# Performance work log

Hardware: AMD Instinct MI355X
Metric: run time of the kernel (lower is better)

Reference implementation:

```python
import jax, jax.numpy as jnp
import numpy as np

D = 256
H = 4
HD = D // H


def rotate_half(x):
    xp = x.reshape(x.shape[:-1] + (-1, 2))
    x1, x2 = xp[..., 0], xp[..., 1]
    return jnp.stack((-x2, x1), axis=-1).reshape(x.shape)


def apply_rope(freqs, t):
    # freqs: [2, B, 1, N, HD]; t: [B, H, N, HD]
    return t * freqs[0] + rotate_half(t) * freqs[1]


def layernorm(x, g, b, eps=1e-5):
    m = jnp.mean(x, axis=-1, keepdims=True)
    v = jnp.var(x, axis=-1, keepdims=True)
    return (x - m) * jax.lax.rsqrt(v + eps) * g + b


def ffn(z, W1, b1, g, be, W2, b2):
    h = layernorm(z @ W1 + b1, g, be)
    h = jax.nn.gelu(h, approximate=False)
    return h @ W2 + b2


def heads_split(t):
    B, N, _ = t.shape
    return t.reshape(B, N, H, HD).transpose(0, 2, 1, 3)  # [B,H,N,HD]


def heads_merge(t):
    B, h, N, hd = t.shape
    return t.transpose(0, 2, 1, 3).reshape(B, N, h * hd)


def sdpa(q, k, v):
    s = q.shape[-1] ** (-0.5)
    sim = jnp.einsum('bhid,bhjd->bhij', q, k) * s
    attn = jax.nn.softmax(sim, axis=-1)
    return jnp.einsum('bhij,bhjd->bhid', attn, v)


def self_block(x, enc, Wqkv, bqkv, Wo, bo, W1, b1, g, be, W2, b2):
    B, N, _ = x.shape
    qkv = (x @ Wqkv + bqkv).reshape(B, N, H, HD, 3).transpose(0, 2, 1, 3, 4)
    q, k, v = qkv[..., 0], qkv[..., 1], qkv[..., 2]
    q = apply_rope(enc, q)
    k = apply_rope(enc, k)
    msg = heads_merge(sdpa(q, k, v)) @ Wo + bo
    return x + ffn(jnp.concatenate([x, msg], axis=-1), W1, b1, g, be, W2, b2)


def cross_block(x0, x1, Wqk, bqk, Wv, bv, Wo, bo, W1, b1, g, be, W2, b2):
    qk0 = heads_split(x0 @ Wqk + bqk)
    qk1 = heads_split(x1 @ Wqk + bqk)
    v0 = heads_split(x0 @ Wv + bv)
    v1 = heads_split(x1 @ Wv + bv)
    s = HD ** (-0.5)
    qk0 = qk0 * (s ** 0.5)
    qk1 = qk1 * (s ** 0.5)
    sim = jnp.einsum('bhid,bhjd->bhij', qk0, qk1)
    attn01 = jax.nn.softmax(sim, axis=-1)
    attn10 = jax.nn.softmax(sim.transpose(0, 1, 3, 2), axis=-1)
    m0 = jnp.einsum('bhij,bhjd->bhid', attn01, v1)
    m1 = jnp.einsum('bhij,bhjd->bhid', attn10, v0)
    m0 = heads_merge(m0) @ Wo + bo
    m1 = heads_merge(m1) @ Wo + bo
    x0 = x0 + ffn(jnp.concatenate([x0, m0], axis=-1), W1, b1, g, be, W2, b2)
    x1 = x1 + ffn(jnp.concatenate([x1, m1], axis=-1), W1, b1, g, be, W2, b2)
    return x0, x1


def setup_inputs() -> dict:
    key = jax.random.key(0)
    ks = jax.random.split(key, 24)
    B, N = 4, 2048
    desc0 = jax.random.normal(ks[0], (B, N, D), jnp.float32)
    desc1 = jax.random.normal(ks[1], (B, N, D), jnp.float32)
    encoding0 = jax.random.uniform(ks[2], (2, B, 1, N, HD), jnp.float32)
    encoding1 = jax.random.uniform(ks[3], (2, B, 1, N, HD), jnp.float32)

    def lin(k, fin, fout):
        k1, k2 = jax.random.split(k)
        W = jax.random.normal(k1, (fin, fout), jnp.float32) * (fin ** -0.5)
        b = jax.random.normal(k2, (fout,), jnp.float32) * 0.01
        return W, b

    Wqkv, bqkv = lin(ks[4], D, 3 * D)
    Wo_s, bo_s = lin(ks[5], D, D)
    W1_s, b1_s = lin(ks[6], 2 * D, 2 * D)
    g_s = jnp.ones((2 * D,), jnp.float32)
    be_s = jnp.zeros((2 * D,), jnp.float32)
    W2_s, b2_s = lin(ks[7], 2 * D, D)
    Wqk_c, bqk_c = lin(ks[8], D, D)
    Wv_c, bv_c = lin(ks[9], D, D)
    Wo_c, bo_c = lin(ks[10], D, D)
    W1_c, b1_c = lin(ks[11], 2 * D, 2 * D)
    g_c = jnp.ones((2 * D,), jnp.float32)
    be_c = jnp.zeros((2 * D,), jnp.float32)
    W2_c, b2_c = lin(ks[12], 2 * D, D)
    return dict(desc0=desc0, desc1=desc1, encoding0=encoding0, encoding1=encoding1,
                Wqkv=Wqkv, bqkv=bqkv, Wo_s=Wo_s, bo_s=bo_s,
                W1_s=W1_s, b1_s=b1_s, g_s=g_s, be_s=be_s, W2_s=W2_s, b2_s=b2_s,
                Wqk_c=Wqk_c, bqk_c=bqk_c, Wv_c=Wv_c, bv_c=bv_c, Wo_c=Wo_c, bo_c=bo_c,
                W1_c=W1_c, b1_c=b1_c, g_c=g_c, be_c=be_c, W2_c=W2_c, b2_c=b2_c)


def reference(desc0, desc1, encoding0, encoding1,
              Wqkv, bqkv, Wo_s, bo_s, W1_s, b1_s, g_s, be_s, W2_s, b2_s,
              Wqk_c, bqk_c, Wv_c, bv_c, Wo_c, bo_c, W1_c, b1_c, g_c, be_c, W2_c, b2_c):
    d0 = self_block(desc0, encoding0, Wqkv, bqkv, Wo_s, bo_s, W1_s, b1_s, g_s, be_s, W2_s, b2_s)
    d1 = self_block(desc1, encoding1, Wqkv, bqkv, Wo_s, bo_s, W1_s, b1_s, g_s, be_s, W2_s, b2_s)
    return cross_block(d0, d1, Wqk_c, bqk_c, Wv_c, bv_c, Wo_c, bo_c, W1_c, b1_c, g_c, be_c, W2_c, b2_c)
```

## Files before the change

### kernel.cpp

```cpp
#include <hip/hip_runtime.h>
#include <math.h>

#define BB 4
#define HH 4
#define NN 2048
#define DD 256
#define HDIM 64
#define NTOK 8192
#define NTOK2 16384

typedef __attribute__((ext_vector_type(8))) __bf16 bf16x8;
typedef __attribute__((ext_vector_type(8))) unsigned short ushort8;
typedef __attribute__((ext_vector_type(4))) float floatx4;
typedef __attribute__((ext_vector_type(4))) short short4v;

union U8 { ushort8 u; bf16x8 b; };
union U4 { unsigned int u[2]; unsigned long long l; short4v s; };

#define MFMA16(a, b, c) __builtin_amdgcn_mfma_f32_16x16x16bf16_1k(a, b, c, 0, 0, 0)

__device__ __forceinline__ unsigned short f2bf(float x) {
    unsigned int u = __float_as_uint(x);
    u += 0x7FFF + ((u >> 16) & 1);
    return (unsigned short)(u >> 16);
}
__device__ __forceinline__ float bf2f(unsigned short u) {
    return __uint_as_float(((unsigned int)u) << 16);
}
__device__ __forceinline__ unsigned int cvtpk(float a, float b) {
    unsigned int r;
    asm("v_cvt_pk_bf16_f32 %0, %1, %2" : "=v"(r) : "v"(a), "v"(b));
    return r;
}
__device__ __forceinline__ floatx4 fmax4(floatx4 a, floatx4 b) {
    floatx4 r;
    r[0] = fmaxf(a[0], b[0]); r[1] = fmaxf(a[1], b[1]);
    r[2] = fmaxf(a[2], b[2]); r[3] = fmaxf(a[3], b[3]);
    return r;
}

struct WTab {
    const float* w[7];
    unsigned short* o[7];
    int K[7];
    int N[7];
    int st[7];
    int t0[8];
};

__global__ __launch_bounds__(256) void wtrans(WTab tab)
{
    __shared__ float lds[32][33];
    const int t = threadIdx.x;
    int bid = blockIdx.x;
    int s = 0;
    while (bid >= tab.t0[s + 1]) s++;
    const int ti = bid - tab.t0[s];
    const int K = tab.K[s], N = tab.N[s], st = tab.st[s];
    const int tx = ti % (N / 32), ty = ti / (N / 32);
    const int k0 = ty * 32, n0 = tx * 32;
    const float* W = tab.w[s];
    unsigned short* Wt = tab.o[s];

    {
        int r = t >> 3, c = (t & 7) * 4;
        float4 a = *(const float4*)&W[(size_t)(k0 + r) * N + n0 + c];
        lds[r][c] = a.x; lds[r][c+1] = a.y; lds[r][c+2] = a.z; lds[r][c+3] = a.w;
    }
    __syncthreads();
    {
        int n = t >> 3, kq = (t & 7) * 4;
        ushort4 p;
        p.x = f2bf(lds[kq+0][n]); p.y = f2bf(lds[kq+1][n]);
        p.z = f2bf(lds[kq+2][n]); p.w = f2bf(lds[kq+3][n]);
        *(ushort4*)&Wt[(size_t)(n0 + n) * st + k0 + kq] = p;
    }
}

__global__ __launch_bounds__(256) void wfuse(
    const float* __restrict__ Wo_s, const float* __restrict__ W1_s,
    unsigned short* __restrict__ o_s,
    const float* __restrict__ Wo_c, const float* __restrict__ W1_c,
    unsigned short* __restrict__ o_c)
{
    __shared__ float wo[32][33];
    __shared__ float w1[32][68];
    const int t = threadIdx.x;
    const int bid = blockIdx.x;
    const int seg = bid >> 6, ti_ = bid & 63;
    const int i0 = (ti_ >> 3) * 32, n0 = (ti_ & 7) * 64;
    const float* Wo  = seg ? Wo_c : Wo_s;
    const float* W1b = (seg ? W1_c : W1_s) + 256 * 512;
    unsigned short* out = seg ? o_c : o_s;
    const int ti = t >> 3, tn = t & 7;

    float acc[8] = {};
    for (int jc = 0; jc < 256; jc += 32) {
        {
            int r = t >> 3, c = (t & 7) * 4;
            *(float4*)&wo[r][c] = *(const float4*)&Wo[(size_t)(i0 + r) * 256 + jc + c];
            int c8 = (t & 7) * 8;
            *(float4*)&w1[r][c8]     = *(const float4*)&W1b[(size_t)(jc + r) * 512 + n0 + c8];
            *(float4*)&w1[r][c8 + 4] = *(const float4*)&W1b[(size_t)(jc + r) * 512 + n0 + c8 + 4];
        }
        __syncthreads();
        #pragma unroll
        for (int j = 0; j < 32; j++) {
            float a = wo[ti][j];
            #pragma unroll
            for (int e = 0; e < 8; e++) acc[e] += a * w1[j][tn * 8 + e];
        }
        __syncthreads();
    }
    #pragma unroll
    for (int e = 0; e < 8; e++)
        out[(size_t)(n0 + tn * 8 + e) * 512 + 256 + i0 + ti] = f2bf(acc[e]);
}

__global__ __launch_bounds__(256) void bfuse(
    const float* bo_s, const float* W1_s, const float* b1_s, float* bs,
    const float* bo_c, const float* W1_c, const float* b1_c, float* bc)
{
    __shared__ float r[4];
    const int bid = blockIdx.x;
    const int seg = bid >> 9, n = bid & 511;
    const float* bo  = seg ? bo_c : bo_s;
    const float* W1b = (seg ? W1_c : W1_s) + 256 * 512;
    const float* b1  = seg ? b1_c : b1_s;
    float* out       = seg ? bc : bs;
    const int j = threadIdx.x;
    float a = bo[j] * W1b[(size_t)j * 512 + n];
    #pragma unroll
    for (int o = 32; o > 0; o >>= 1) a += __shfl_xor(a, o, 64);
    if ((j & 63) == 0) r[j >> 6] = a;
    __syncthreads();
    if (j == 0) out[n] = b1[n] + r[0] + r[1] + r[2] + r[3];
}

__global__ __launch_bounds__(256) void gemm_mfma(
    const unsigned short* __restrict__ A, int lda,
    const unsigned short* __restrict__ Wt, int K,
    const float* __restrict__ bias, const float* __restrict__ bias2, int mode,
    float* outF, unsigned short* outH0, unsigned short* outH1,
    unsigned short* outH2,
    int ldc, const float* R0, const float* R1)
{
    __shared__ __align__(16) unsigned short As[64 * 72];
    __shared__ __align__(16) unsigned short Bs[128 * 72];
    const int t = threadIdx.x;
    const int w = t >> 6, lane = t & 63, quad = lane >> 4, l15 = lane & 15;
    const int m0 = blockIdx.y * 64, n0 = blockIdx.x * 128;
    const int wn = w * 32;
    const int sar = t >> 2, sac = (t & 3) * 16;
    const int sbr = t >> 1, sbc = (t & 1) * 32;

    const unsigned short* Ap = A  + (size_t)(m0 + sar) * lda + sac;
    const unsigned short* Bp = Wt + (size_t)(n0 + sbr) * K   + sbc;

    ushort8 pa0 = *(const ushort8*)(Ap);
    ushort8 pa1 = *(const ushort8*)(Ap + 8);
    ushort8 pb0 = *(const ushort8*)(Bp);
    ushort8 pb1 = *(const ushort8*)(Bp + 8);
    ushort8 pb2 = *(const ushort8*)(Bp + 16);
    ushort8 pb3 = *(const ushort8*)(Bp + 24);

    floatx4 acc[4][2];
    #pragma unroll
    for (int i = 0; i < 4; i++)
        #pragma unroll
        for (int j = 0; j < 2; j++) acc[i][j] = (floatx4){0.f, 0.f, 0.f, 0.f};

    const int nk = K >> 6;
    for (int kk = 0; kk < nk; kk++) {
        *(ushort8*)&As[sar * 72 + sac]      = pa0;
        *(ushort8*)&As[sar * 72 + sac + 8]  = pa1;
        *(ushort8*)&Bs[sbr * 72 + sbc]      = pb0;
        *(ushort8*)&Bs[sbr * 72 + sbc + 8]  = pb1;
        *(ushort8*)&Bs[sbr * 72 + sbc + 16] = pb2;
        *(ushort8*)&Bs[sbr * 72 + sbc + 24] = pb3;
        __syncthreads();
        if (kk + 1 < nk) {
            int ko = (kk + 1) * 64;
            pa0 = *(const ushort8*)(Ap + ko);
            pa1 = *(const ushort8*)(Ap + ko + 8);
            pb0 = *(const ushort8*)(Bp + ko);
            pb1 = *(const ushort8*)(Bp + ko + 8);
            pb2 = *(const ushort8*)(Bp + ko + 16);
            pb3 = *(const ushort8*)(Bp + ko + 24);
        }
        #pragma unroll
        for (int kh = 0; kh < 2; kh++) {
            U8 af[4], bf[2];
            #pragma unroll
            for (int i = 0; i < 4; i++)
                af[i].u = *(const ushort8*)&As[(i * 16 + l15) * 72 + kh * 32 + quad * 8];
            #pragma unroll
            for (int j = 0; j < 2; j++)
                bf[j].u = *(const ushort8*)&Bs[(wn + j * 16 + l15) * 72 + kh * 32 + quad * 8];
            #pragma unroll
            for (int i = 0; i < 4; i++)
                #pragma unroll
                for (int j = 0; j < 2; j++)
                    acc[i][j] = __builtin_amdgcn_mfma_f32_16x16x32_bf16(af[i].b, bf[j].b, acc[i][j], 0, 0, 0);
        }
        __syncthreads();
    }

    #pragma unroll
    for (int i = 0; i < 4; i++) {
        #pragma unroll
        for (int j = 0; j < 2; j++) {
            int col = n0 + wn + j * 16 + l15;
            float bv = (mode == 2 && col >= 256) ? bias2[col & 255] : bias[col];
            #pragma unroll
            for (int r = 0; r < 4; r++) {
                int grow = m0 + i * 16 + quad * 4 + r;
                float v = acc[i][j][r] + bv;
                if (mode == 1) {
                    outH0[(size_t)grow * ldc + col] = f2bf(v);
                } else if (mode == 2) {
                    int cc = col & 255;
                    int h = cc >> 6, d = cc & 63;
                    int ds = grow >> 13, b = (grow >> 11) & 3, n = grow & 2047;
                    int bh = ds * 16 + b * 4 + h;
                    if (col < 256)
                        outH0[((size_t)bh * NN + n) * HDIM + d] = f2bf(v);
                    else
                        outH1[((size_t)bh * HDIM + d) * NN + n] = f2bf(v);
                } else if (mode == 3) {
                    int sel = col % 3, cc = col / 3;
                    int h = cc >> 6, d = cc & 63;
                    int ds = grow >> 13, b = (grow >> 11) & 3, n = grow & 2047;
                    int bh = ds * 16 + b * 4 + h;
                    if (sel == 0)
                        outH0[((size_t)bh * NN + n) * HDIM + d] = f2bf(v);
                    else if (sel == 1)
                        outH1[((size_t)bh * NN + n) * HDIM + d] = f2bf(v);
                    else
                        outH2[((size_t)bh * HDIM + d) * NN + n] = f2bf(v);
                } else {
                    const float* R = (grow < NTOK) ? R0 : R1;
                    float vv = v + R[(size_t)(grow & 8191) * 256 + col];
                    outF[(size_t)grow * 256 + col] = vv;
                    if (outH0) outH0[(size_t)grow * 256 + col] = f2bf(vv);
                    if (outH1) outH1[(size_t)grow * 512 + col] = f2bf(vv);
                }
            }
        }
    }
}

__global__ __launch_bounds__(256) void rope_k(unsigned short* __restrict__ qb,
                                              unsigned short* __restrict__ kb,
                                              const float* __restrict__ enc0,
                                              const float* __restrict__ enc1)
{
    int i = blockIdx.x * 256 + threadIdx.x;
    int dp = (i & 31) * 2;
    int n  = (i >> 5) & (NN - 1);
    int h  = (i >> 16) & 3;
    int b  = (i >> 18) & 3;
    int ds = (i >> 20) & 1;
    int bf = (i >> 21) & 1;
    unsigned short* tq = (bf ? kb : qb) +
        (((size_t)(ds * 16 + b * 4 + h)) * NN + n) * HDIM + dp;
    const float* e0 = (ds ? enc1 : enc0) + ((size_t)b * NN + n) * HDIM + dp;
    const float* e1 = e0 + (size_t)BB * NN * HDIM;
    float x0 = bf2f(tq[0]), x1 = bf2f(tq[1]);
    float y0 = x0 * e0[0] - x1 * e1[0];
    float y1 = x1 * e0[1] + x0 * e1[1];
    tq[0] = f2bf(y0); tq[1] = f2bf(y1);
}

__global__ __launch_bounds__(256) void flash_attn(
    const unsigned short* __restrict__ Q, const unsigned short* __restrict__ K,
    const unsigned short* __restrict__ V, unsigned short* __restrict__ O,
    int ldo, int kvx, float qscale)
{
    __shared__ __align__(16) unsigned short Ks[2][64 * 72];
    __shared__ __align__(16) unsigned short Vt[2][64 * 72];

    const int t    = threadIdx.x;
    const int w    = t >> 6;
    const int lane = t & 63;
    const int quad = lane >> 4;
    const int l15  = lane & 15;
    const int bh   = blockIdx.y;
    const int kbh  = bh ^ kvx;
    const int q0   = blockIdx.x * 128;

    const unsigned short* Qb  = Q + (size_t)bh  * NN * HDIM;
    const unsigned short* Kb  = K + (size_t)kbh * NN * HDIM;
    const unsigned short* VTb = V + (size_t)kbh * NN * HDIM;

    const int srf = t >> 3, scf = (t & 7) * 8;

    bf16x8 qf0[2], qf1[2];
    #pragma unroll
    for (int i = 0; i < 2; i++) {
        const int qrow = q0 + w * 32 + i * 16 + l15;
        U8 r0, r1, x0, x1;
        r0.u = *(const ushort8*)&Qb[(size_t)qrow * HDIM + quad * 8];
        r1.u = *(const ushort8*)&Qb[(size_t)qrow * HDIM + 32 + quad * 8];
        #pragma unroll
        for (int j = 0; j < 8; j++) {
            x0.u[j] = f2bf(bf2f(r0.u[j]) * qscale);
            x1.u[j] = f2bf(bf2f(r1.u[j]) * qscale);
        }
        qf0[i] = x0.b; qf1[i] = x1.b;
    }

    floatx4 o[2][4];
    #pragma unroll
    for (int i = 0; i < 2; i++)
        #pragma unroll
        for (int c = 0; c < 4; c++) o[i][c] = (floatx4){0.f, 0.f, 0.f, 0.f};
    float m[2] = {-1e30f, -1e30f};
    float l[2] = {0.f, 0.f};

    ushort8 ka0 = *(const ushort8*)&Kb[(size_t)srf * HDIM + scf];
    ushort8 ka1 = *(const ushort8*)&Kb[(size_t)(srf + 32) * HDIM + scf];
    ushort8 va0 = *(const ushort8*)&VTb[(size_t)srf * NN + scf];
    ushort8 va1 = *(const ushort8*)&VTb[(size_t)(srf + 32) * NN + scf];
    *(ushort8*)&Ks[0][srf * 72 + scf]        = ka0;
    *(ushort8*)&Ks[0][(srf + 32) * 72 + scf] = ka1;
    *(ushort8*)&Vt[0][srf * 72 + scf]        = va0;
    *(ushort8*)&Vt[0][(srf + 32) * 72 + scf] = va1;
    __syncthreads();

    int cur = 0;
    for (int j0 = 0; j0 < NN; j0 += 64, cur ^= 1) {
        const int more = (j0 + 64 < NN);
        if (more) {
            const int jn = j0 + 64;
            ka0 = *(const ushort8*)&Kb[(size_t)(jn + srf) * HDIM + scf];
            ka1 = *(const ushort8*)&Kb[(size_t)(jn + srf + 32) * HDIM + scf];
            va0 = *(const ushort8*)&VTb[(size_t)srf * NN + jn + scf];
            va1 = *(const ushort8*)&VTb[(size_t)(srf + 32) * NN + jn + scf];
        }

        floatx4 s[2][4];
        __builtin_amdgcn_s_setprio(1);
        #pragma unroll
        for (int t4 = 0; t4 < 4; t4++) {
            U8 k0, k1;
            k0.u = *(const ushort8*)&Ks[cur][(t4 * 16 + l15) * 72 + quad * 8];
            k1.u = *(const ushort8*)&Ks[cur][(t4 * 16 + l15) * 72 + 32 + quad * 8];
            #pragma unroll
            for (int i = 0; i < 2; i++) {
                floatx4 z = (floatx4){0.f, 0.f, 0.f, 0.f};
                z = __builtin_amdgcn_mfma_f32_16x16x32_bf16(k0.b, qf0[i], z, 0, 0, 0);
                z = __builtin_amdgcn_mfma_f32_16x16x32_bf16(k1.b, qf1[i], z, 0, 0, 0);
                s[i][t4] = z;
            }
        }
        __builtin_amdgcn_s_setprio(0);

        short4v pf[2][4];
        #pragma unroll
        for (int i = 0; i < 2; i++) {
            floatx4 a = fmax4(fmax4(s[i][0], s[i][1]), fmax4(s[i][2], s[i][3]));
            float mx = fmaxf(fmaxf(a[0], a[1]), fmaxf(a[2], a[3]));
            mx = fmaxf(mx, __shfl_xor(mx, 16, 64));
            mx = fmaxf(mx, __shfl_xor(mx, 32, 64));
            if (!__all(mx <= m[i] + 8.f)) {
                float mn = fmaxf(m[i], mx);
                float al = exp2f(m[i] - mn);
                m[i] = mn;
                l[i] *= al;
                #pragma unroll
                for (int c = 0; c < 4; c++)
                    #pragma unroll
                    for (int r = 0; r < 4; r++) o[i][c][r] *= al;
            }
            float rs = 0.f;
            #pragma unroll
            for (int t4 = 0; t4 < 4; t4++)
                #pragma unroll
                for (int r = 0; r < 4; r++) {
                    float p = exp2f(s[i][t4][r] - m[i]);
                    s[i][t4][r] = p;
                    rs += p;
                }
            rs += __shfl_xor(rs, 16, 64);
            rs += __shfl_xor(rs, 32, 64);
            l[i] += rs;

            #pragma unroll
            for (int t4 = 0; t4 < 4; t4++) {
                U4 pk;
                pk.u[0] = cvtpk(s[i][t4][0], s[i][t4][1]);
                pk.u[1] = cvtpk(s[i][t4][2], s[i][t4][3]);
                pf[i][t4] = pk.s;
            }
        }

        __builtin_amdgcn_s_setprio(1);
        #pragma unroll
        for (int c = 0; c < 4; c++) {
            U4 vf[4];
            #pragma unroll
            for (int t4 = 0; t4 < 4; t4++)
                vf[t4].l = *(const unsigned long long*)
                    &Vt[cur][(c * 16 + l15) * 72 + t4 * 16 + quad * 4];
            #pragma unroll
            for (int i = 0; i < 2; i++)
                #pragma unroll
                for (int t4 = 0; t4 < 4; t4++)
                    o[i][c] = MFMA16(vf[t4].s, pf[i][t4], o[i][c]);
        }
        __builtin_amdgcn_s_setprio(0);

        if (more) {
            *(ushort8*)&Ks[cur ^ 1][srf * 72 + scf]        = ka0;
            *(ushort8*)&Ks[cur ^ 1][(srf + 32) * 72 + scf] = ka1;
            *(ushort8*)&Vt[cur ^ 1][srf * 72 + scf]        = va0;
            *(ushort8*)&Vt[cur ^ 1][(srf + 32) * 72 + scf] = va1;
            __syncthreads();
        }
    }

    const int ds = bh >> 4, b = (bh >> 2) & 3, h = bh & 3;
    #pragma unroll
    for (int i = 0; i < 2; i++) {
        const int q = q0 + w * 32 + i * 16 + l15;
        const size_t row = (size_t)ds * NTOK + b * NN + q;
        float inv = 1.f / l[i];
        #pragma unroll
        for (int c = 0; c < 4; c++) {
            U4 pk;
            pk.u[0] = cvtpk(o[i][c][0] * inv, o[i][c][1] * inv);
            pk.u[1] = cvtpk(o[i][c][2] * inv, o[i][c][3] * inv);
            *(unsigned long long*)&O[row * ldo + h * HDIM + c * 16 + quad * 4] = pk.l;
        }
    }
}

__global__ __launch_bounds__(256) void ln_gelu(
    unsigned short* __restrict__ hb, const float* __restrict__ g,
    const float* __restrict__ be)
{
    const int lane = threadIdx.x & 63;
    const int wv   = threadIdx.x >> 6;
    const size_t row = (size_t)blockIdx.x * 4 + wv;
    unsigned short* ip = hb + row * 512 + lane * 8;
    U8 v; v.u = *(const ushort8*)ip;
    float x[8];
    float s = 0.f, ss = 0.f;
    #pragma unroll
    for (int j = 0; j < 8; j++) {
        x[j] = bf2f(v.u[j]);
        s += x[j];
        ss += x[j] * x[j];
    }
    #pragma unroll
    for (int o = 32; o > 0; o >>= 1) {
        s  += __shfl_xor(s, o, 64);
        ss += __shfl_xor(ss, o, 64);
    }
    float mean = s * (1.f / 512.f);
    float var  = ss * (1.f / 512.f) - mean * mean;
    float inv  = rsqrtf(var + 1e-5f);
    float4 g0 = *(const float4*)&g[lane * 8];
    float4 g1 = *(const float4*)&g[lane * 8 + 4];
    float4 b0 = *(const float4*)&be[lane * 8];
    float4 b1 = *(const float4*)&be[lane * 8 + 4];
    float gg[8] = {g0.x, g0.y, g0.z, g0.w, g1.x, g1.y, g1.z, g1.w};
    float bb[8] = {b0.x, b0.y, b0.z, b0.w, b1.x, b1.y, b1.z, b1.w};
    #pragma unroll
    for (int j = 0; j < 8; j++) {
        float y = (x[j] - mean) * inv * gg[j] + bb[j];
        v.u[j] = f2bf(0.5f * y * (1.f + erff(y * 0.70710678f)));
    }
    *(ushort8*)ip = v.u;
}

__global__ __launch_bounds__(256) void copy_to_cat(
    const float* __restrict__ s0, const float* __restrict__ s1,
    unsigned short* __restrict__ cat)
{
    int i = blockIdx.x * 256 + threadIdx.x;
    int row = i >> 6, c4 = (i & 63) * 4;
    const float* s = (row < NTOK) ? s0 : s1;
    float4 a = *(const float4*)&s[(size_t)(row & 8191) * 256 + c4];
    ushort4 p = { f2bf(a.x), f2bf(a.y), f2bf(a.z), f2bf(a.w) };
    *(ushort4*)&cat[(size_t)row * 512 + c4] = p;
}

extern "C" void kernel_launch(void* const* d_in, const int* in_sizes, int n_in,
                              void* d_out, int out_size, void* d_ws, size_t ws_size,
                              hipStream_t stream)
{
    const float* desc0 = (const float*)d_in[0];
    const float* desc1 = (const float*)d_in[1];
    const float* enc0  = (const float*)d_in[2];
    const float* enc1  = (const float*)d_in[3];
    const float* Wqkv  = (const float*)d_in[4];  const float* bqkv  = (const float*)d_in[5];
    const float* Wo_s  = (const float*)d_in[6];  const float* bo_s  = (const float*)d_in[7];
    const float* W1_s  = (const float*)d_in[8];  const float* b1_s  = (const float*)d_in[9];
    const float* g_s   = (const float*)d_in[10]; const float* be_s  = (const float*)d_in[11];
    const float* W2_s  = (const float*)d_in[12]; const float* b2_s  = (const float*)d_in[13];
    const float* Wqk_c = (const float*)d_in[14]; const float* bqk_c = (const float*)d_in[15];
    const float* Wv_c  = (const float*)d_in[16]; const float* bv_c  = (const float*)d_in[17];
    const float* Wo_c  = (const float*)d_in[18]; const float* bo_c  = (const float*)d_in[19];
    const float* W1_c  = (const float*)d_in[20]; const float* b1_c  = (const float*)d_in[21];
    const float* g_c   = (const float*)d_in[22]; const float* be_c  = (const float*)d_in[23];
    const float* W2_c  = (const float*)d_in[24]; const float* b2_c  = (const float*)d_in[25];

    char* ws = (char*)d_ws;
    unsigned short* wt  = (unsigned short*)ws;
    unsigned short* qb  = (unsigned short*)(ws + 2490368);
    unsigned short* kb  = (unsigned short*)(ws + 10878976);
    unsigned short* vb  = (unsigned short*)(ws + 27656192);
    unsigned short* cat = (unsigned short*)(ws + 36044800);
    unsigned short* hb  = (unsigned short*)(ws + 52822016);
    unsigned short* dbf = (unsigned short*)(ws + 86376448);

    unsigned short* t_qkv  = wt;
    float*          bias_s = (float*)(wt + 196608);
    unsigned short* t_w1s  = wt + 262144;
    unsigned short* t_w2s  = wt + 524288;
    unsigned short* t_wqkc = wt + 655360;
    float*          bias_c = (float*)(wt + 786432);
    unsigned short* t_w1c  = wt + 851968;
    unsigned short* t_w2c  = wt + 1114112;

    float* outF = (float*)d_out;

    dim3 blk(256);

    WTab tab;
    tab.w[0] = Wqkv;  tab.o[0] = t_qkv;          tab.K[0] = 256; tab.N[0] = 768; tab.st[0] = 256;
    tab.w[1] = W1_s;  tab.o[1] = t_w1s;          tab.K[1] = 256; tab.N[1] = 512; tab.st[1] = 512;
    tab.w[2] = W2_s;  tab.o[2] = t_w2s;          tab.K[2] = 512; tab.N[2] = 256; tab.st[2] = 512;
    tab.w[3] = Wqk_c; tab.o[3] = t_wqkc;         tab.K[3] = 256; tab.N[3] = 256; tab.st[3] = 256;
    tab.w[4] = Wv_c;  tab.o[4] = t_wqkc + 65536; tab.K[4] = 256; tab.N[4] = 256; tab.st[4] = 256;
    tab.w[5] = W1_c;  tab.o[5] = t_w1c;          tab.K[5] = 256; tab.N[5] = 512; tab.st[5] = 512;
    tab.w[6] = W2_c;  tab.o[6] = t_w2c;          tab.K[6] = 512; tab.N[6] = 256; tab.st[6] = 512;
    int acc_t = 0;
    for (int s = 0; s < 7; s++) {
        tab.t0[s] = acc_t;
        acc_t += (tab.K[s] / 32) * (tab.N[s] / 32);
    }
    tab.t0[7] = acc_t;
    hipLaunchKernelGGL(wtrans, dim3(acc_t), blk, 0, stream, tab);
    hipLaunchKernelGGL(wfuse, dim3(128), blk, 0, stream,
                       Wo_s, W1_s, t_w1s, Wo_c, W1_c, t_w1c);
    hipLaunchKernelGGL(bfuse, dim3(1024), blk, 0, stream,
                       bo_s, W1_s, b1_s, bias_s, bo_c, W1_c, b1_c, bias_c);

    auto gemm = [&](const unsigned short* A, int lda, const unsigned short* Wtp,
                    int K, const float* bias, const float* bias2, int Nc, int mode,
                    float* oF, unsigned short* oh0, unsigned short* oh1,
                    unsigned short* oh2, int ldc, const float* r0, const float* r1) {
        dim3 g(Nc / 128, NTOK2 / 64);
        hipLaunchKernelGGL(gemm_mfma, g, blk, 0, stream,
                           A, lda, Wtp, K, bias, bias2, mode,
                           oF, oh0, oh1, oh2, ldc, r0, r1);
    };

    const float QS = 0.125f * 1.44269504088896f;

    hipLaunchKernelGGL(copy_to_cat, dim3(4096), blk, 0, stream, desc0, desc1, cat);
    gemm(cat, 512, t_qkv, 256, bqkv, nullptr, 768, 3,
         nullptr, qb, kb, vb, 0, nullptr, nullptr);
    hipLaunchKernelGGL(rope_k, dim3(16384), blk, 0, stream, qb, kb, enc0, enc1);
    hipLaunchKernelGGL(flash_attn, dim3(NN / 128, 32), blk, 0, stream,
                       qb, kb, vb, cat + 256, 512, 0, QS);
    gemm(cat, 512, t_w1s, 512, bias_s, nullptr, 512, 1,
         nullptr, hb, nullptr, nullptr, 512, nullptr, nullptr);
    hipLaunchKernelGGL(ln_gelu, dim3(NTOK2 / 4), blk, 0, stream, hb, g_s, be_s);
    gemm(hb, 512, t_w2s, 512, b2_s, nullptr, 256, 4,
         outF, dbf, cat, nullptr, 256, desc0, desc1);

    gemm(dbf, 256, t_wqkc, 256, bqk_c, bv_c, 512, 2,
         nullptr, qb, vb, nullptr, 0, nullptr, nullptr);
    hipLaunchKernelGGL(flash_attn, dim3(NN / 128, 32), blk, 0, stream,
                       qb, qb, vb, cat + 256, 512, 16, QS);
    gemm(cat, 512, t_w1c, 512, bias_c, nullptr, 512, 1,
         nullptr, hb, nullptr, nullptr, 512, nullptr, nullptr);
    hipLaunchKernelGGL(ln_gelu, dim3(NTOK2 / 4), blk, 0, stream, hb, g_c, be_c);
    gemm(hb, 512, t_w2c, 512, b2_c, nullptr, 256, 4,
         outF, nullptr, nullptr, nullptr, 256, outF, outF + (size_t)NTOK * 256);
}
```

Baseline: 460.6 us.

## Fuse RoPE into QKV GEMM epilogue via permuted weight columns

Permutes the QKV weight columns during transposition so q, k and v occupy contiguous 256-column blocks. The GEMM epilogue can then apply rotary embedding in registers, taking the pair partner with a lane shuffle, and write rotated bf16 q/k directly. This removes the separate rope kernel, which re-read and re-wrote all of q and k. In exchange a dedicated weight-permute kernel is added, and the epilogue now gathers the bias and loads encodings per element.

```diff
diff --git a/kernel.cpp b/kernel.cpp
--- a/kernel.cpp
+++ b/kernel.cpp
@@ -74,6 +74,31 @@
         p.x = f2bf(lds[kq+0][n]); p.y = f2bf(lds[kq+1][n]);
         p.z = f2bf(lds[kq+2][n]); p.w = f2bf(lds[kq+3][n]);
         *(ushort4*)&Wt[(size_t)(n0 + n) * st + k0 + kq] = p;
+    }
+}
+
+__global__ __launch_bounds__(256) void qkv_trans(
+    const float* __restrict__ W, unsigned short* __restrict__ Wt)
+{
+    __shared__ float lds[32][33];
+    const int t = threadIdx.x;
+    const int p0 = blockIdx.x * 32, k0 = blockIdx.y * 32;
+    {
+        int r = t >> 3, c = (t & 7) * 4;
+        #pragma unroll
+        for (int u = 0; u < 4; u++) {
+            int p = p0 + c + u;
+            int src = ((p >> 6) & 3) * 192 + (p & 63) * 3 + (p >> 8);
+            lds[r][c + u] = W[(size_t)(k0 + r) * 768 + src];
+        }
+    }
+    __syncthreads();
+    {
+        int n = t >> 3, kq = (t & 7) * 4;
+        ushort4 pk;
+        pk.x = f2bf(lds[kq+0][n]); pk.y = f2bf(lds[kq+1][n]);
+        pk.z = f2bf(lds[kq+2][n]); pk.w = f2bf(lds[kq+3][n]);
+        *(ushort4*)&Wt[(size_t)(p0 + n) * 256 + k0 + kq] = pk;
     }
 }
 
@@ -211,7 +236,11 @@
         #pragma unroll
         for (int j = 0; j < 2; j++) {
             int col = n0 + wn + j * 16 + l15;
-            float bv = (mode == 2 && col >= 256) ? bias2[col & 255] : bias[col];
+            float bv;
+            if (mode == 2 && col >= 256) bv = bias2[col & 255];
+            else if (mode == 3)
+                bv = bias[((col >> 6) & 3) * 192 + (col & 63) * 3 + (col >> 8)];
+            else bv = bias[col];
             #pragma unroll
             for (int r = 0; r < 4; r++) {
                 int grow = m0 + i * 16 + quad * 4 + r;
@@ -228,16 +257,22 @@
                     else
                         outH1[((size_t)bh * HDIM + d) * NN + n] = f2bf(v);
                 } else if (mode == 3) {
-                    int sel = col % 3, cc = col / 3;
-                    int h = cc >> 6, d = cc & 63;
+                    int sel = col >> 8, cc2 = col & 255;
+                    int h = cc2 >> 6, d = cc2 & 63;
                     int ds = grow >> 13, b = (grow >> 11) & 3, n = grow & 2047;
                     int bh = ds * 16 + b * 4 + h;
-                    if (sel == 0)
-                        outH0[((size_t)bh * NN + n) * HDIM + d] = f2bf(v);
-                    else if (sel == 1)
-                        outH1[((size_t)bh * NN + n) * HDIM + d] = f2bf(v);
-                    else
+                    if (sel == 2) {
                         outH2[((size_t)bh * HDIM + d) * NN + n] = f2bf(v);
+                    } else {
+                        float prt = __shfl_xor(v, 1, 64);
+                        const float* e = (ds ? R1 : R0)
+                            + ((size_t)b * NN + n) * HDIM + d;
+                        float e0v = e[0], e1v = e[BB * NN * HDIM];
+                        float y = (d & 1) ? v * e0v + prt * e1v
+                                          : v * e0v - prt * e1v;
+                        unsigned short* op = sel ? outH1 : outH0;
+                        op[((size_t)bh * NN + n) * HDIM + d] = f2bf(y);
+                    }
                 } else {
                     const float* R = (grow < NTOK) ? R0 : R1;
                     float vv = v + R[(size_t)(grow & 8191) * 256 + col];
@@ -248,28 +283,6 @@
             }
         }
     }
-}
-
-__global__ __launch_bounds__(256) void rope_k(unsigned short* __restrict__ qb,
-                                              unsigned short* __restrict__ kb,
-                                              const float* __restrict__ enc0,
-                                              const float* __restrict__ enc1)
-{
-    int i = blockIdx.x * 256 + threadIdx.x;
-    int dp = (i & 31) * 2;
-    int n  = (i >> 5) & (NN - 1);
-    int h  = (i >> 16) & 3;
-    int b  = (i >> 18) & 3;
-    int ds = (i >> 20) & 1;
-    int bf = (i >> 21) & 1;
-    unsigned short* tq = (bf ? kb : qb) +
-        (((size_t)(ds * 16 + b * 4 + h)) * NN + n) * HDIM + dp;
-    const float* e0 = (ds ? enc1 : enc0) + ((size_t)b * NN + n) * HDIM + dp;
-    const float* e1 = e0 + (size_t)BB * NN * HDIM;
-    float x0 = bf2f(tq[0]), x1 = bf2f(tq[1]);
-    float y0 = x0 * e0[0] - x1 * e1[0];
-    float y1 = x1 * e0[1] + x0 * e1[1];
-    tq[0] = f2bf(y0); tq[1] = f2bf(y1);
 }
 
 __global__ __launch_bounds__(256) void flash_attn(
@@ -529,19 +542,21 @@
 
     dim3 blk(256);
 
+    hipLaunchKernelGGL(qkv_trans, dim3(24, 8), blk, 0, stream, Wqkv, t_qkv);
+
     WTab tab;
-    tab.w[0] = Wqkv;  tab.o[0] = t_qkv;          tab.K[0] = 256; tab.N[0] = 768; tab.st[0] = 256;
-    tab.w[1] = W1_s;  tab.o[1] = t_w1s;          tab.K[1] = 256; tab.N[1] = 512; tab.st[1] = 512;
-    tab.w[2] = W2_s;  tab.o[2] = t_w2s;          tab.K[2] = 512; tab.N[2] = 256; tab.st[2] = 512;
-    tab.w[3] = Wqk_c; tab.o[3] = t_wqkc;         tab.K[3] = 256; tab.N[3] = 256; tab.st[3] = 256;
-    tab.w[4] = Wv_c;  tab.o[4] = t_wqkc + 65536; tab.K[4] = 256; tab.N[4] = 256; tab.st[4] = 256;
-    tab.w[5] = W1_c;  tab.o[5] = t_w1c;          tab.K[5] = 256; tab.N[5] = 512; tab.st[5] = 512;
-    tab.w[6] = W2_c;  tab.o[6] = t_w2c;          tab.K[6] = 512; tab.N[6] = 256; tab.st[6] = 512;
+    tab.w[0] = W1_s;  tab.o[0] = t_w1s;          tab.K[0] = 256; tab.N[0] = 512; tab.st[0] = 512;
+    tab.w[1] = W2_s;  tab.o[1] = t_w2s;          tab.K[1] = 512; tab.N[1] = 256; tab.st[1] = 512;
+    tab.w[2] = Wqk_c; tab.o[2] = t_wqkc;         tab.K[2] = 256; tab.N[2] = 256; tab.st[2] = 256;
+    tab.w[3] = Wv_c;  tab.o[3] = t_wqkc + 65536; tab.K[3] = 256; tab.N[3] = 256; tab.st[3] = 256;
+    tab.w[4] = W1_c;  tab.o[4] = t_w1c;          tab.K[4] = 256; tab.N[4] = 512; tab.st[4] = 512;
+    tab.w[5] = W2_c;  tab.o[5] = t_w2c;          tab.K[5] = 512; tab.N[5] = 256; tab.st[5] = 512;
     int acc_t = 0;
-    for (int s = 0; s < 7; s++) {
+    for (int s = 0; s < 6; s++) {
         tab.t0[s] = acc_t;
         acc_t += (tab.K[s] / 32) * (tab.N[s] / 32);
     }
+    tab.t0[6] = acc_t;
     tab.t0[7] = acc_t;
     hipLaunchKernelGGL(wtrans, dim3(acc_t), blk, 0, stream, tab);
     hipLaunchKernelGGL(wfuse, dim3(128), blk, 0, stream,
@@ -563,8 +578,7 @@
 
     hipLaunchKernelGGL(copy_to_cat, dim3(4096), blk, 0, stream, desc0, desc1, cat);
     gemm(cat, 512, t_qkv, 256, bqkv, nullptr, 768, 3,
-         nullptr, qb, kb, vb, 0, nullptr, nullptr);
-    hipLaunchKernelGGL(rope_k, dim3(16384), blk, 0, stream, qb, kb, enc0, enc1);
+         nullptr, qb, kb, vb, 0, enc0, enc1);
     hipLaunchKernelGGL(flash_attn, dim3(NN / 128, 32), blk, 0, stream,
                        qb, kb, vb, cat + 256, 512, 0, QS);
     gemm(cat, 512, t_w1s, 512, bias_s, nullptr, 512, 1,
```

After: 470.5 us. +2.2%, slower.
